# Kernel tuning notes

Measured on AMD Instinct MI355X. Metric: run time of the kernel, lower is better.

## Reference

```python
import jax, jax.numpy as jnp
import numpy as np

DIM = 512
HEADS = 8
DH = DIM // HEADS
SCALE = DH ** -0.5
LN_EPS = 1e-5


def setup_inputs() -> dict:
    key = jax.random.key(0)
    ks = jax.random.split(key, 6)
    b, n = 16, 1024
    x = jax.random.normal(ks[0], (b, n, DIM), dtype=jnp.float32)
    # to_qkv: Linear(dim, 3*dim, bias=False)
    Wqkv = jax.random.normal(ks[1], (DIM, 3 * DIM), dtype=jnp.float32) * (DIM ** -0.5)
    # LayerNorm(inner_dim) affine params
    ln_g = jnp.ones((DIM,), dtype=jnp.float32)
    ln_b = jnp.zeros((DIM,), dtype=jnp.float32)
    # to_out: Linear(inner_dim, dim) with bias
    Wo = jax.random.normal(ks[2], (DIM, DIM), dtype=jnp.float32) * (DIM ** -0.5)
    bo = jnp.zeros((DIM,), dtype=jnp.float32)
    return {"x": x, "Wqkv": Wqkv, "ln_g": ln_g, "ln_b": ln_b, "Wo": Wo, "bo": bo}


def reference(x, Wqkv, ln_g, ln_b, Wo, bo):
    b, n, d = x.shape
    h, dh = HEADS, DH
    qkv = x @ Wqkv                              # [b, n, 3d]
    q, k, v = jnp.split(qkv, 3, axis=-1)        # each [b, n, d]
    def to_heads(t):
        return t.reshape(b, n, h, dh).transpose(0, 2, 1, 3)  # [b, h, n, dh]
    q, k, v = to_heads(q), to_heads(k), to_heads(v)
    dots = jnp.einsum('bhid,bhjd->bhij', q, k) * SCALE       # [b, h, n, n]
    attn = jax.nn.relu(dots)                                 # ReLU instead of softmax
    out = jnp.einsum('bhij,bhjd->bhid', attn, v)             # [b, h, n, dh]
    out = out.transpose(0, 2, 1, 3).reshape(b, n, d)         # [b, n, d]
    # LayerNorm over last dim
    mu = jnp.mean(out, axis=-1, keepdims=True)
    var = jnp.var(out, axis=-1, keepdims=True)
    out = (out - mu) * jax.lax.rsqrt(var + LN_EPS) * ln_g + ln_b
    return out @ Wo + bo
```

## Files before the change

kernel.cpp:

```cpp
#include <hip/hip_runtime.h>
#include <cstdint>
#include <cstddef>

typedef unsigned short u16;
typedef float f32x4 __attribute__((ext_vector_type(4)));
typedef short short8 __attribute__((ext_vector_type(8)));
typedef u16 u16x4 __attribute__((ext_vector_type(4)));

#define MFMA_BF16(acc, a, b) \
  asm("v_mfma_f32_16x16x32_bf16 %0, %1, %2, %0" : "+v"(acc) : "v"(a), "v"(b))

#define GLDS16(gp, lp) __builtin_amdgcn_global_load_lds( \
    (__attribute__((address_space(1))) void*)(void*)(uintptr_t)(gp), \
    (__attribute__((address_space(3))) void*)(lp), 16, 0, 0)

static __device__ __forceinline__ u16 f2bf(float f) {
  union { float f; unsigned u; } x; x.f = f;
  unsigned u = x.u + 0x7fffu + ((x.u >> 16) & 1u);
  return (u16)(u >> 16);
}

__global__ __launch_bounds__(256) void cvt_kernel(const float* __restrict__ src,
                                                  u16* __restrict__ dst, int n4) {
  int stride = gridDim.x * 256;
  for (int i = blockIdx.x * 256 + threadIdx.x; i < n4; i += stride) {
    f32x4 v = ((const f32x4*)src)[i];
    u16x4 o;
    o[0] = f2bf(v[0]); o[1] = f2bf(v[1]); o[2] = f2bf(v[2]); o[3] = f2bf(v[3]);
    ((u16x4*)dst)[i] = o;
  }
}

__global__ __launch_bounds__(256) void tcvt_kernel(const float* __restrict__ src,
                                                   u16* __restrict__ dst, int R, int C,
                                                   int sclim) {
  __shared__ float tile[64][65];
  int c0 = blockIdx.x * 64, r0 = blockIdx.y * 64;
  for (int t = threadIdx.x; t < 4096; t += 256) {
    int r = t >> 6, c = t & 63;
    tile[r][c] = src[(size_t)(r0 + r) * C + c0 + c];
  }
  __syncthreads();
  for (int t = threadIdx.x; t < 4096; t += 256) {
    int rr = t >> 6, cc = t & 63;
    float sc = (c0 + rr) < sclim ? 0.125f : 1.0f;
    dst[(size_t)(c0 + rr) * R + r0 + cc] = f2bf(tile[cc][rr] * sc);
  }
}

__global__ __launch_bounds__(256) void gemm_qkv_kernel(const u16* __restrict__ A,
                                                       const u16* __restrict__ BT,
                                                       u16* __restrict__ qk,
                                                       u16* __restrict__ vT) {
  __shared__ u16 As[128 * 64];
  __shared__ u16 Bs[128 * 64];
  const int tid = threadIdx.x, lane = tid & 63, wave = tid >> 6;
  const int wr = wave >> 1, wc = wave & 1;
  const int m0 = blockIdx.y * 128, n0 = blockIdx.x * 128;
  f32x4 acc[4][4] = {};
  for (int kt = 0; kt < 8; ++kt) {
    int k0 = kt * 64;
    __syncthreads();
    #pragma unroll
    for (int t = 0; t < 4; ++t) {
      int ch = wave * 4 + t;
      GLDS16(A + (size_t)(m0 + ch * 8 + (lane >> 3)) * 512 + k0 + (lane & 7) * 8, &As[ch * 512]);
      GLDS16(BT + (size_t)(n0 + ch * 8 + (lane >> 3)) * 512 + k0 + (lane & 7) * 8, &Bs[ch * 512]);
    }
    __syncthreads();
    #pragma unroll
    for (int kk = 0; kk < 2; ++kk) {
      short8 af[4], bfr[4];
      #pragma unroll
      for (int m = 0; m < 4; ++m)
        af[m] = *(const short8*)&As[(wr * 64 + m * 16 + (lane & 15)) * 64 + kk * 32 + (lane >> 4) * 8];
      #pragma unroll
      for (int n = 0; n < 4; ++n)
        bfr[n] = *(const short8*)&Bs[(wc * 64 + n * 16 + (lane & 15)) * 64 + kk * 32 + (lane >> 4) * 8];
      #pragma unroll
      for (int m = 0; m < 4; ++m)
        #pragma unroll
        for (int n = 0; n < 4; ++n)
          MFMA_BF16(acc[m][n], af[m], bfr[n]);
    }
  }
  const int row0 = m0 + wr * 64, col0 = n0 + wc * 64;
  if (n0 < 1024) {
    #pragma unroll
    for (int m = 0; m < 4; ++m) {
      int row = row0 + m * 16 + (lane >> 4) * 4;
      #pragma unroll
      for (int n = 0; n < 4; ++n) {
        int col = col0 + n * 16 + (lane & 15);
        #pragma unroll
        for (int i = 0; i < 4; ++i)
          qk[(size_t)(row + i) * 1024 + col] = f2bf(acc[m][n][i]);
      }
    }
  } else {
    #pragma unroll
    for (int m = 0; m < 4; ++m) {
      int row = row0 + m * 16 + (lane >> 4) * 4;
      int bb = row >> 10, nn = row & 1023;
      #pragma unroll
      for (int n = 0; n < 4; ++n) {
        int d = col0 + n * 16 + (lane & 15) - 1024;
        u16x4 pk;
        #pragma unroll
        for (int i = 0; i < 4; ++i) pk[i] = f2bf(acc[m][n][i]);
        *(u16x4*)&vT[(size_t)(bb * 512 + d) * 1024 + nn] = pk;
      }
    }
  }
}

__global__ __launch_bounds__(256) void attn_kernel(const u16* __restrict__ qk,
                                                   const u16* __restrict__ vT,
                                                   float* __restrict__ aout) {
  __shared__ u16 smem[24576];
  u16* Ks = smem;
  u16* Ss = smem;
  u16* Vs = smem + 16384;
  const int tid = threadIdx.x, lane = tid & 63, wave = tid >> 6;
  const int wr = wave >> 1, wc = wave & 1;
  const int L = blockIdx.x;
  const int qt = L >> 7, bh = L & 127, h = bh & 7, b = bh >> 3;
  const size_t qrow0 = (size_t)b * 1024 + qt * 128;

  short8 qf[4][2];
  #pragma unroll
  for (int m = 0; m < 4; ++m)
    #pragma unroll
    for (int kk = 0; kk < 2; ++kk)
      qf[m][kk] = *(const short8*)&qk[(qrow0 + wr * 64 + m * 16 + (lane & 15)) * 1024
                                      + h * 64 + kk * 32 + (lane >> 4) * 8];
  f32x4 acc[4][2] = {};
  for (int jt = 0; jt < 8; ++jt) {
    __syncthreads();
    const u16* Kg = qk + ((size_t)b * 1024 + jt * 128) * 1024 + 512 + h * 64;
    const u16* Vg = vT + ((size_t)b * 512 + h * 64) * 1024 + jt * 128;
    #pragma unroll
    for (int t = 0; t < 4; ++t) {
      int ch = wave * 4 + t;
      GLDS16(Kg + (size_t)(ch * 8 + (lane >> 3)) * 1024 + ((lane & 7) ^ (lane >> 3)) * 8,
             &Ks[ch * 512]);
      GLDS16(Vg + (size_t)(ch * 4 + (lane >> 4)) * 1024 + ((lane & 15) ^ (t * 4 + (lane >> 4))) * 8,
             &Vs[ch * 512]);
    }
    __syncthreads();
    f32x4 sacc[4][4] = {};
    __builtin_amdgcn_s_setprio(1);
    #pragma unroll
    for (int kk = 0; kk < 2; ++kk) {
      short8 kf[4];
      #pragma unroll
      for (int n = 0; n < 4; ++n) {
        int r = wc * 64 + n * 16 + (lane & 15);
        int slot = kk * 4 + (lane >> 4);
        kf[n] = *(const short8*)&Ks[r * 64 + ((slot ^ (r & 7)) * 8)];
      }
      #pragma unroll
      for (int n = 0; n < 4; ++n)
        #pragma unroll
        for (int m = 0; m < 4; ++m)
          MFMA_BF16(sacc[n][m], kf[n], qf[m][kk]);
    }
    __builtin_amdgcn_s_setprio(0);
    __syncthreads();
    #pragma unroll
    for (int m = 0; m < 4; ++m) {
      int i = wr * 64 + m * 16 + (lane & 15);
      unsigned rowbase = (unsigned)i * 256;
      unsigned sw = (unsigned)(i & 15) << 4;
      #pragma unroll
      for (int n = 0; n < 4; ++n) {
        int j0 = wc * 64 + n * 16 + (lane >> 4) * 4;
        u16x4 pk;
        #pragma unroll
        for (int r = 0; r < 4; ++r) pk[r] = f2bf(fmaxf(sacc[n][m][r], 0.f));
        *(u16x4*)((char*)Ss + (rowbase + (((unsigned)j0 * 2) ^ sw))) = pk;
      }
    }
    __syncthreads();
    __builtin_amdgcn_s_setprio(1);
    #pragma unroll
    for (int ks = 0; ks < 4; ++ks) {
      short8 sa[4], vb[2];
      #pragma unroll
      for (int m = 0; m < 4; ++m) {
        int i = wr * 64 + m * 16 + (lane & 15);
        unsigned c2 = (unsigned)(ks * 32 + (lane >> 4) * 8) * 2;
        sa[m] = *(const short8*)((const char*)Ss + (unsigned)i * 256 + (c2 ^ ((unsigned)(i & 15) << 4)));
      }
      #pragma unroll
      for (int n = 0; n < 2; ++n) {
        int r = wc * 32 + n * 16 + (lane & 15);
        int slot = ks * 4 + (lane >> 4);
        vb[n] = *(const short8*)&Vs[r * 128 + ((slot ^ (r & 15)) * 8)];
      }
      #pragma unroll
      for (int m = 0; m < 4; ++m)
        #pragma unroll
        for (int n = 0; n < 2; ++n)
          MFMA_BF16(acc[m][n], sa[m], vb[n]);
    }
    __builtin_amdgcn_s_setprio(0);
  }
  #pragma unroll
  for (int m = 0; m < 4; ++m) {
    int row = wr * 64 + m * 16 + (lane >> 4) * 4;
    #pragma unroll
    for (int n = 0; n < 2; ++n) {
      int col = h * 64 + wc * 32 + n * 16 + (lane & 15);
      #pragma unroll
      for (int i = 0; i < 4; ++i)
        aout[(qrow0 + row + i) * 512 + col] = acc[m][n][i];
    }
  }
}

__global__ __launch_bounds__(256) void ln_kernel(const float* __restrict__ x,
                                                 const float* __restrict__ g,
                                                 const float* __restrict__ bt,
                                                 u16* __restrict__ y) {
  const int lane = threadIdx.x & 63, wave = threadIdx.x >> 6;
  const size_t row = (size_t)blockIdx.x * 4 + wave;
  const float* xr = x + row * 512;
  f32x4 v0 = *(const f32x4*)&xr[lane * 4];
  f32x4 v1 = *(const f32x4*)&xr[256 + lane * 4];
  float s = v0[0] + v0[1] + v0[2] + v0[3] + v1[0] + v1[1] + v1[2] + v1[3];
  float q = v0[0]*v0[0] + v0[1]*v0[1] + v0[2]*v0[2] + v0[3]*v0[3]
          + v1[0]*v1[0] + v1[1]*v1[1] + v1[2]*v1[2] + v1[3]*v1[3];
  #pragma unroll
  for (int o = 32; o > 0; o >>= 1) { s += __shfl_xor(s, o); q += __shfl_xor(q, o); }
  float mean = s * (1.f / 512.f);
  float var  = q * (1.f / 512.f) - mean * mean;
  float rstd = rsqrtf(var + 1e-5f);
  f32x4 g0 = *(const f32x4*)&g[lane * 4],  g1 = *(const f32x4*)&g[256 + lane * 4];
  f32x4 b0 = *(const f32x4*)&bt[lane * 4], b1 = *(const f32x4*)&bt[256 + lane * 4];
  u16x4 o0, o1;
  #pragma unroll
  for (int i = 0; i < 4; ++i) {
    o0[i] = f2bf((v0[i] - mean) * rstd * g0[i] + b0[i]);
    o1[i] = f2bf((v1[i] - mean) * rstd * g1[i] + b1[i]);
  }
  *(u16x4*)&y[row * 512 + lane * 4] = o0;
  *(u16x4*)&y[row * 512 + 256 + lane * 4] = o1;
}

__global__ __launch_bounds__(256) void gemm_out_kernel(const u16* __restrict__ A,
                                                       const u16* __restrict__ BT,
                                                       const float* __restrict__ bias,
                                                       float* __restrict__ out) {
  __shared__ u16 As[128 * 64];
  __shared__ u16 Bs[128 * 64];
  const int tid = threadIdx.x, lane = tid & 63, wave = tid >> 6;
  const int wr = wave >> 1, wc = wave & 1;
  const int m0 = blockIdx.y * 128, n0 = blockIdx.x * 128;
  f32x4 acc[4][4] = {};
  for (int kt = 0; kt < 8; ++kt) {
    int k0 = kt * 64;
    __syncthreads();
    #pragma unroll
    for (int t = 0; t < 4; ++t) {
      int ch = wave * 4 + t;
      GLDS16(A + (size_t)(m0 + ch * 8 + (lane >> 3)) * 512 + k0 + (lane & 7) * 8, &As[ch * 512]);
      GLDS16(BT + (size_t)(n0 + ch * 8 + (lane >> 3)) * 512 + k0 + (lane & 7) * 8, &Bs[ch * 512]);
    }
    __syncthreads();
    #pragma unroll
    for (int kk = 0; kk < 2; ++kk) {
      short8 af[4], bfr[4];
      #pragma unroll
      for (int m = 0; m < 4; ++m)
        af[m] = *(const short8*)&As[(wr * 64 + m * 16 + (lane & 15)) * 64 + kk * 32 + (lane >> 4) * 8];
      #pragma unroll
      for (int n = 0; n < 4; ++n)
        bfr[n] = *(const short8*)&Bs[(wc * 64 + n * 16 + (lane & 15)) * 64 + kk * 32 + (lane >> 4) * 8];
      #pragma unroll
      for (int m = 0; m < 4; ++m)
        #pragma unroll
        for (int n = 0; n < 4; ++n)
          MFMA_BF16(acc[m][n], af[m], bfr[n]);
    }
  }
  const int row0 = m0 + wr * 64, col0 = n0 + wc * 64;
  #pragma unroll
  for (int m = 0; m < 4; ++m) {
    int row = row0 + m * 16 + (lane >> 4) * 4;
    #pragma unroll
    for (int n = 0; n < 4; ++n) {
      int col = col0 + n * 16 + (lane & 15);
      float bv = bias[col];
      #pragma unroll
      for (int i = 0; i < 4; ++i)
        out[(size_t)(row + i) * 512 + col] = acc[m][n][i] + bv;
    }
  }
}

extern "C" void kernel_launch(void* const* d_in, const int* in_sizes, int n_in,
                              void* d_out, int out_size, void* d_ws, size_t ws_size,
                              hipStream_t stream) {
  const float* x    = (const float*)d_in[0];
  const float* Wqkv = (const float*)d_in[1];
  const float* ln_g = (const float*)d_in[2];
  const float* ln_b = (const float*)d_in[3];
  const float* Wo   = (const float*)d_in[4];
  const float* bo   = (const float*)d_in[5];
  float* out = (float*)d_out;
  char* ws = (char*)d_ws;

  u16*   xbf   = (u16*)(ws);
  u16*   wqkvt = (u16*)(ws + 16777216);
  u16*   wot   = (u16*)(ws + 18350080);
  u16*   qkb   = (u16*)(ws + 18874368);
  u16*   vtb   = (u16*)(ws + 52428800);
  float* att   = (float*)(ws + 69206016);

  cvt_kernel<<<4096, 256, 0, stream>>>(x, xbf, 8388608 / 4);
  tcvt_kernel<<<dim3(24, 8), 256, 0, stream>>>(Wqkv, wqkvt, 512, 1536, 512);
  tcvt_kernel<<<dim3(8, 8), 256, 0, stream>>>(Wo, wot, 512, 512, 0);
  gemm_qkv_kernel<<<dim3(12, 128), 256, 0, stream>>>(xbf, wqkvt, qkb, vtb);
  attn_kernel<<<1024, 256, 0, stream>>>(qkb, vtb, att);
  ln_kernel<<<4096, 256, 0, stream>>>(att, ln_g, ln_b, xbf);
  gemm_out_kernel<<<dim3(4, 128), 256, 0, stream>>>(xbf, wot, bo, out);
}
```

Measured before the change: 137.2 us.

## Double-buffer K/V tiles and keep ReLU scores in registers via shuffles

Restructures the attention kernel so each wave owns 32 query rows and walks 64-key tiles, with the next K/V tile prefetched into a second LDS buffer while the current one is computed. The ReLU scores are no longer written to and re-read from shared memory. They are packed to bf16 with v_cvt_pk_bf16_f32 and rearranged across lanes with shuffles to form the A operand of the PV MFMA. This removes the score round trip through LDS and two barriers per tile, at the cost of twice as many loop iterations, extra shuffle instructions, and smaller per-wave tiles.

```diff
diff --git a/kernel.cpp b/kernel.cpp
--- a/kernel.cpp
+++ b/kernel.cpp
@@ -6,6 +6,7 @@
 typedef float f32x4 __attribute__((ext_vector_type(4)));
 typedef short short8 __attribute__((ext_vector_type(8)));
 typedef u16 u16x4 __attribute__((ext_vector_type(4)));
+typedef unsigned u32x4 __attribute__((ext_vector_type(4)));
 
 #define MFMA_BF16(acc, a, b) \
   asm("v_mfma_f32_16x16x32_bf16 %0, %1, %2, %0" : "+v"(acc) : "v"(a), "v"(b))
@@ -117,106 +118,109 @@
 __global__ __launch_bounds__(256) void attn_kernel(const u16* __restrict__ qk,
                                                    const u16* __restrict__ vT,
                                                    float* __restrict__ aout) {
-  __shared__ u16 smem[24576];
-  u16* Ks = smem;
-  u16* Ss = smem;
-  u16* Vs = smem + 16384;
+  __shared__ u16 smem[16384];
   const int tid = threadIdx.x, lane = tid & 63, wave = tid >> 6;
-  const int wr = wave >> 1, wc = wave & 1;
+  const int g = lane >> 4, lo = lane & 15;
+  const int krow = lane >> 3, kslot = lane & 7;
   const int L = blockIdx.x;
   const int qt = L >> 7, bh = L & 127, h = bh & 7, b = bh >> 3;
   const size_t qrow0 = (size_t)b * 1024 + qt * 128;
-
-  short8 qf[4][2];
-  #pragma unroll
-  for (int m = 0; m < 4; ++m)
+  const u16* Kg0 = qk + (size_t)b * 1024 * 1024 + 512 + h * 64;
+  const u16* Vg0 = vT + ((size_t)b * 512 + h * 64) * 1024;
+
+  short8 qf[2][2];
+  #pragma unroll
+  for (int m = 0; m < 2; ++m)
     #pragma unroll
     for (int kk = 0; kk < 2; ++kk)
-      qf[m][kk] = *(const short8*)&qk[(qrow0 + wr * 64 + m * 16 + (lane & 15)) * 1024
-                                      + h * 64 + kk * 32 + (lane >> 4) * 8];
-  f32x4 acc[4][2] = {};
-  for (int jt = 0; jt < 8; ++jt) {
-    __syncthreads();
-    const u16* Kg = qk + ((size_t)b * 1024 + jt * 128) * 1024 + 512 + h * 64;
-    const u16* Vg = vT + ((size_t)b * 512 + h * 64) * 1024 + jt * 128;
-    #pragma unroll
-    for (int t = 0; t < 4; ++t) {
-      int ch = wave * 4 + t;
-      GLDS16(Kg + (size_t)(ch * 8 + (lane >> 3)) * 1024 + ((lane & 7) ^ (lane >> 3)) * 8,
-             &Ks[ch * 512]);
-      GLDS16(Vg + (size_t)(ch * 4 + (lane >> 4)) * 1024 + ((lane & 15) ^ (t * 4 + (lane >> 4))) * 8,
-             &Vs[ch * 512]);
-    }
-    __syncthreads();
-    f32x4 sacc[4][4] = {};
+      qf[m][kk] = *(const short8*)&qk[(qrow0 + wave * 32 + m * 16 + lo) * 1024
+                                      + h * 64 + kk * 32 + g * 8];
+
+  const int srcA = ((g & 1) * 2) * 16 + lo;
+  const int srcB = srcA + 16;
+
+  f32x4 acc[2][4] = {};
+
+  #pragma unroll
+  for (int t = 0; t < 2; ++t) {
+    int ch = wave * 2 + t;
+    GLDS16(Kg0 + (size_t)(ch * 8 + krow) * 1024 + (kslot ^ krow) * 8, &smem[ch * 512]);
+    GLDS16(Vg0 + (size_t)(ch * 8 + krow) * 1024 + (kslot ^ krow) * 8, &smem[4096 + ch * 512]);
+  }
+  int cur = 0;
+  for (int jt = 0; jt < 16; ++jt) {
+    __syncthreads();
+    if (jt < 15) {
+      const u16* Kg = Kg0 + (size_t)(jt + 1) * 64 * 1024;
+      const u16* Vg = Vg0 + (jt + 1) * 64;
+      u16* nb = &smem[(cur ^ 1) * 8192];
+      #pragma unroll
+      for (int t = 0; t < 2; ++t) {
+        int ch = wave * 2 + t;
+        GLDS16(Kg + (size_t)(ch * 8 + krow) * 1024 + (kslot ^ krow) * 8, &nb[ch * 512]);
+        GLDS16(Vg + (size_t)(ch * 8 + krow) * 1024 + (kslot ^ krow) * 8, &nb[4096 + ch * 512]);
+      }
+    }
+    const u16* Ks = &smem[cur * 8192];
+    const u16* Vs = &smem[cur * 8192 + 4096];
+    f32x4 sacc[4][2] = {};
     __builtin_amdgcn_s_setprio(1);
     #pragma unroll
-    for (int kk = 0; kk < 2; ++kk) {
-      short8 kf[4];
+    for (int kk = 0; kk < 2; ++kk)
       #pragma unroll
       for (int n = 0; n < 4; ++n) {
-        int r = wc * 64 + n * 16 + (lane & 15);
-        int slot = kk * 4 + (lane >> 4);
-        kf[n] = *(const short8*)&Ks[r * 64 + ((slot ^ (r & 7)) * 8)];
-      }
-      #pragma unroll
-      for (int n = 0; n < 4; ++n)
-        #pragma unroll
-        for (int m = 0; m < 4; ++m)
-          MFMA_BF16(sacc[n][m], kf[n], qf[m][kk]);
-    }
+        int r = n * 16 + lo;
+        short8 kf = *(const short8*)&Ks[r * 64 + (((kk * 4 + g) ^ (lo & 7)) * 8)];
+        #pragma unroll
+        for (int m = 0; m < 2; ++m)
+          MFMA_BF16(sacc[n][m], kf, qf[m][kk]);
+      }
     __builtin_amdgcn_s_setprio(0);
-    __syncthreads();
-    #pragma unroll
-    for (int m = 0; m < 4; ++m) {
-      int i = wr * 64 + m * 16 + (lane & 15);
-      unsigned rowbase = (unsigned)i * 256;
-      unsigned sw = (unsigned)(i & 15) << 4;
-      #pragma unroll
-      for (int n = 0; n < 4; ++n) {
-        int j0 = wc * 64 + n * 16 + (lane >> 4) * 4;
-        u16x4 pk;
-        #pragma unroll
-        for (int r = 0; r < 4; ++r) pk[r] = f2bf(fmaxf(sacc[n][m][r], 0.f));
-        *(u16x4*)((char*)Ss + (rowbase + (((unsigned)j0 * 2) ^ sw))) = pk;
-      }
-    }
-    __syncthreads();
+    unsigned pk[4][2][2];
+    #pragma unroll
+    for (int n = 0; n < 4; ++n)
+      #pragma unroll
+      for (int m = 0; m < 2; ++m) {
+        float a0 = fmaxf(sacc[n][m][0], 0.f), a1 = fmaxf(sacc[n][m][1], 0.f);
+        float a2 = fmaxf(sacc[n][m][2], 0.f), a3 = fmaxf(sacc[n][m][3], 0.f);
+        asm("v_cvt_pk_bf16_f32 %0, %1, %2" : "=v"(pk[n][m][0]) : "v"(a0), "v"(a1));
+        asm("v_cvt_pk_bf16_f32 %0, %1, %2" : "=v"(pk[n][m][1]) : "v"(a2), "v"(a3));
+      }
     __builtin_amdgcn_s_setprio(1);
     #pragma unroll
-    for (int ks = 0; ks < 4; ++ks) {
-      short8 sa[4], vb[2];
-      #pragma unroll
-      for (int m = 0; m < 4; ++m) {
-        int i = wr * 64 + m * 16 + (lane & 15);
-        unsigned c2 = (unsigned)(ks * 32 + (lane >> 4) * 8) * 2;
-        sa[m] = *(const short8*)((const char*)Ss + (unsigned)i * 256 + (c2 ^ ((unsigned)(i & 15) << 4)));
-      }
-      #pragma unroll
-      for (int n = 0; n < 2; ++n) {
-        int r = wc * 32 + n * 16 + (lane & 15);
-        int slot = ks * 4 + (lane >> 4);
-        vb[n] = *(const short8*)&Vs[r * 128 + ((slot ^ (r & 15)) * 8)];
-      }
-      #pragma unroll
-      for (int m = 0; m < 4; ++m)
-        #pragma unroll
-        for (int n = 0; n < 2; ++n)
-          MFMA_BF16(acc[m][n], sa[m], vb[n]);
+    for (int c = 0; c < 2; ++c) {
+      u32x4 paw[2];
+      #pragma unroll
+      for (int m = 0; m < 2; ++m)
+        #pragma unroll
+        for (int w = 0; w < 4; ++w) {
+          int src = (w >> 1) ? srcB : srcA;
+          unsigned tA = (unsigned)__shfl((int)pk[2 * c][m][w & 1], src);
+          unsigned tB = (unsigned)__shfl((int)pk[2 * c + 1][m][w & 1], src);
+          paw[m][w] = (g >> 1) ? tB : tA;
+        }
+      #pragma unroll
+      for (int t = 0; t < 4; ++t) {
+        int d = t * 16 + lo;
+        short8 vb = *(const short8*)&Vs[d * 64 + (((c * 4 + g) ^ (lo & 7)) * 8)];
+        #pragma unroll
+        for (int m = 0; m < 2; ++m) {
+          short8 pa = *(short8*)&paw[m];
+          MFMA_BF16(acc[m][t], pa, vb);
+        }
+      }
     }
     __builtin_amdgcn_s_setprio(0);
-  }
-  #pragma unroll
-  for (int m = 0; m < 4; ++m) {
-    int row = wr * 64 + m * 16 + (lane >> 4) * 4;
-    #pragma unroll
-    for (int n = 0; n < 2; ++n) {
-      int col = h * 64 + wc * 32 + n * 16 + (lane & 15);
-      #pragma unroll
-      for (int i = 0; i < 4; ++i)
-        aout[(qrow0 + row + i) * 512 + col] = acc[m][n][i];
-    }
-  }
+    cur ^= 1;
+  }
+  #pragma unroll
+  for (int m = 0; m < 2; ++m)
+    #pragma unroll
+    for (int t = 0; t < 4; ++t)
+      #pragma unroll
+      for (int r = 0; r < 4; ++r)
+        aout[(qrow0 + wave * 32 + m * 16 + g * 4 + r) * 512 + h * 64 + t * 16 + lo]
+            = acc[m][t][r];
 }
 
 __global__ __launch_bounds__(256) void ln_kernel(const float* __restrict__ x,
```

Result: no change. 138.9 us (+1.3%).

## Stage V-transpose epilogue through LDS and swizzle GEMM block order for XCDs

Applied to the files above, without the earlier changes.

The QKV GEMM's transposed V output is first staged in shared memory, with a padded stride, so that global writes become contiguous rows of vT instead of scattered 8-byte writes. Both GEMMs switch to a 1D grid and remap block IDs so that blocks landing on the same XCD (bid mod 8) work on contiguous tile ranges, which should improve L2 reuse of A and B. This adds a shared-memory round trip and extra barriers in the V epilogue.

```diff
diff --git a/kernel.cpp b/kernel.cpp
--- a/kernel.cpp
+++ b/kernel.cpp
@@ -52,11 +52,15 @@
                                                        const u16* __restrict__ BT,
                                                        u16* __restrict__ qk,
                                                        u16* __restrict__ vT) {
-  __shared__ u16 As[128 * 64];
-  __shared__ u16 Bs[128 * 64];
+  __shared__ u16 smem[16896];
+  u16* As = smem;
+  u16* Bs = smem + 8192;
   const int tid = threadIdx.x, lane = tid & 63, wave = tid >> 6;
   const int wr = wave >> 1, wc = wave & 1;
-  const int m0 = blockIdx.y * 128, n0 = blockIdx.x * 128;
+  const int bid = blockIdx.x;
+  const int lin = (bid & 7) * 192 + (bid >> 3);
+  const int my = lin / 12, nx = lin - my * 12;
+  const int m0 = my * 128, n0 = nx * 128;
   f32x4 acc[4][4] = {};
   for (int kt = 0; kt < 8; ++kt) {
     int k0 = kt * 64;
@@ -98,18 +102,26 @@
       }
     }
   } else {
+    __syncthreads();
+    const int lo = lane & 15, g = lane >> 4;
     #pragma unroll
     for (int m = 0; m < 4; ++m) {
-      int row = row0 + m * 16 + (lane >> 4) * 4;
-      int bb = row >> 10, nn = row & 1023;
+      int tl0 = wr * 64 + m * 16 + g * 4;
       #pragma unroll
       for (int n = 0; n < 4; ++n) {
-        int d = col0 + n * 16 + (lane & 15) - 1024;
+        int dl = wc * 64 + n * 16 + lo;
         u16x4 pk;
         #pragma unroll
         for (int i = 0; i < 4; ++i) pk[i] = f2bf(acc[m][n][i]);
-        *(u16x4*)&vT[(size_t)(bb * 512 + d) * 1024 + nn] = pk;
-      }
+        *(u16x4*)&smem[dl * 132 + tl0] = pk;
+      }
+    }
+    __syncthreads();
+    const int bb = m0 >> 10, nn0 = m0 & 1023, d0 = n0 - 1024;
+    for (int t = tid; t < 128 * 32; t += 256) {
+      int d = t >> 5, sg = t & 31;
+      u16x4 v = *(const u16x4*)&smem[d * 132 + sg * 4];
+      *(u16x4*)&vT[(size_t)(bb * 512 + d0 + d) * 1024 + nn0 + sg * 4] = v;
     }
   }
 }
@@ -256,7 +268,9 @@
   __shared__ u16 Bs[128 * 64];
   const int tid = threadIdx.x, lane = tid & 63, wave = tid >> 6;
   const int wr = wave >> 1, wc = wave & 1;
-  const int m0 = blockIdx.y * 128, n0 = blockIdx.x * 128;
+  const int bid = blockIdx.x;
+  const int lin = (bid & 7) * 64 + (bid >> 3);
+  const int m0 = (lin >> 2) * 128, n0 = (lin & 3) * 128;
   f32x4 acc[4][4] = {};
   for (int kt = 0; kt < 8; ++kt) {
     int k0 = kt * 64;
@@ -321,8 +335,8 @@
   cvt_kernel<<<4096, 256, 0, stream>>>(x, xbf, 8388608 / 4);
   tcvt_kernel<<<dim3(24, 8), 256, 0, stream>>>(Wqkv, wqkvt, 512, 1536, 512);
   tcvt_kernel<<<dim3(8, 8), 256, 0, stream>>>(Wo, wot, 512, 512, 0);
-  gemm_qkv_kernel<<<dim3(12, 128), 256, 0, stream>>>(xbf, wqkvt, qkb, vtb);
+  gemm_qkv_kernel<<<1536, 256, 0, stream>>>(xbf, wqkvt, qkb, vtb);
   attn_kernel<<<1024, 256, 0, stream>>>(qkb, vtb, att);
   ln_kernel<<<4096, 256, 0, stream>>>(att, ln_g, ln_b, xbf);
-  gemm_out_kernel<<<dim3(4, 128), 256, 0, stream>>>(xbf, wot, bo, out);
-}
+  gemm_out_kernel<<<512, 256, 0, stream>>>(xbf, wot, bo, out);
+}
```

Result: faster. 130.8 us (-4.6%).
